# Kernel optimization log

Hardware: AMD Instinct MI355X
Metric: run time of the kernel (lower is better)

## Reference

```python
import jax, jax.numpy as jnp
import numpy as np

N_NODES = 50000
N_EDGES = 800000
N_GRAPHS = 8
IN_CH = 32
HID = 64
EDGE_F = 16
EPS = 1e-5


def setup_inputs() -> dict:
    key = jax.random.key(0)
    ks = jax.random.split(key, 40)
    r = lambda i, shape, s=0.1: (jax.random.normal(ks[i], shape, dtype=jnp.float32) * s)
    inp = {
        "x": jax.random.normal(ks[0], (N_NODES, IN_CH), dtype=jnp.float32),
        "edge_index": jax.random.randint(ks[1], (2, N_EDGES), 0, N_NODES),
        "edge_attr": jax.random.normal(ks[2], (N_EDGES, EDGE_F), dtype=jnp.float32),
        "batch": jnp.sort(jax.random.randint(ks[3], (N_NODES,), 0, N_GRAPHS)),
        "nt_w": r(4, (IN_CH, HID)), "nt_b": jnp.zeros((HID,), jnp.float32),
        "ln0_w": jnp.ones((HID,), jnp.float32), "ln0_b": jnp.zeros((HID,), jnp.float32),
        "c1_wl": r(5, (HID, 2 * HID)), "c1_bl": jnp.zeros((2 * HID,), jnp.float32),
        "c1_wr": r(6, (HID, 2 * HID)), "c1_br": jnp.zeros((2 * HID,), jnp.float32),
        "c1_we": r(7, (EDGE_F, 2 * HID)), "c1_att": r(8, (2, HID)),
        "c1_b": jnp.zeros((2 * HID,), jnp.float32),
        "n1_w": jnp.ones((2 * HID,), jnp.float32), "n1_b": jnp.zeros((2 * HID,), jnp.float32),
        "c2_wl": r(9, (2 * HID, 2 * HID)), "c2_bl": jnp.zeros((2 * HID,), jnp.float32),
        "c2_wr": r(10, (2 * HID, 2 * HID)), "c2_br": jnp.zeros((2 * HID,), jnp.float32),
        "c2_we": r(11, (EDGE_F, 2 * HID)), "c2_att": r(12, (2, HID)),
        "c2_b": jnp.zeros((2 * HID,), jnp.float32),
        "n2_w": jnp.ones((2 * HID,), jnp.float32), "n2_b": jnp.zeros((2 * HID,), jnp.float32),
        "c3_wl": r(13, (2 * HID, HID)), "c3_bl": jnp.zeros((HID,), jnp.float32),
        "c3_wr": r(14, (2 * HID, HID)), "c3_br": jnp.zeros((HID,), jnp.float32),
        "c3_we": r(15, (EDGE_F, HID)), "c3_att": r(16, (1, HID)),
        "c3_b": jnp.zeros((HID,), jnp.float32),
        "pof_w": r(17, (HID, 1)), "pof_b": jnp.zeros((1,), jnp.float32),
        "hp_w": r(18, (HID, 1)), "hp_b": jnp.zeros((1,), jnp.float32),
    }
    return inp


def _layer_norm(x, w, b):
    # torch nn.LayerNorm over last dim
    mu = jnp.mean(x, axis=-1, keepdims=True)
    xc = x - mu
    var = jnp.mean(xc * xc, axis=-1, keepdims=True)
    return xc * jax.lax.rsqrt(var + EPS) * w + b


def _graph_norm(x, w, b):
    # PyG LayerNorm mode='graph' with batch=None: normalize over all nodes+channels
    mu = jnp.mean(x)
    xc = x - mu
    var = jnp.mean(xc * xc)
    return xc * jax.lax.rsqrt(var + EPS) * w + b


def _gatv2(x, src, dst, ea, wl, bl, wr, br, we, att, b, heads, outc):
    n = x.shape[0]
    xl = (x @ wl + bl).reshape(n, heads, outc)   # source transform
    xr = (x @ wr + br).reshape(n, heads, outc)   # target transform
    e = (ea @ we).reshape(-1, heads, outc)       # [E,H,C] edge embedding
    m = jax.nn.leaky_relu(xl[src] + xr[dst] + e, 0.2)  # [E,H,C]
    alpha = jnp.einsum("ehc,hc->eh", m, att)      # [E,H]
    amax = jax.ops.segment_max(alpha, dst, num_segments=n)
    amax = jnp.where(jnp.isfinite(amax), amax, 0.0)
    p = jnp.exp(alpha - amax[dst])
    denom = jax.ops.segment_sum(p, dst, num_segments=n)
    alpha = p / (denom[dst] + 1e-16)
    out = jax.ops.segment_sum(xl[src] * alpha[..., None], dst, num_segments=n)
    return out.reshape(n, heads * outc) + b


def reference(x, edge_index, edge_attr, batch,
              nt_w, nt_b, ln0_w, ln0_b,
              c1_wl, c1_bl, c1_wr, c1_br, c1_we, c1_att, c1_b, n1_w, n1_b,
              c2_wl, c2_bl, c2_wr, c2_br, c2_we, c2_att, c2_b, n2_w, n2_b,
              c3_wl, c3_bl, c3_wr, c3_br, c3_we, c3_att, c3_b,
              pof_w, pof_b, hp_w, hp_b):
    src, dst = edge_index[0], edge_index[1]
    # node_transform (dropout = identity in eval mode)
    h = _layer_norm(jax.nn.elu(x @ nt_w + nt_b), ln0_w, ln0_b)
    h = _gatv2(h, src, dst, edge_attr, c1_wl, c1_bl, c1_wr, c1_br, c1_we, c1_att, c1_b, 2, HID)
    h = jax.nn.elu(_graph_norm(h, n1_w, n1_b))
    h = _gatv2(h, src, dst, edge_attr, c2_wl, c2_bl, c2_wr, c2_br, c2_we, c2_att, c2_b, 2, HID)
    h = jax.nn.elu(_graph_norm(h, n2_w, n2_b))
    h = _gatv2(h, src, dst, edge_attr, c3_wl, c3_bl, c3_wr, c3_br, c3_we, c3_att, c3_b, 1, HID)
    pof_pred = (h @ pof_w + pof_b)[:, 0]
    sums = jax.ops.segment_sum(h, batch, num_segments=N_GRAPHS)
    cnt = jax.ops.segment_sum(jnp.ones((h.shape[0],), h.dtype), batch, num_segments=N_GRAPHS)
    graph_emb = sums / jnp.maximum(cnt, 1.0)[:, None]
    has_pof_pred = (graph_emb @ hp_w + hp_b)[:, 0]
    return pof_pred, has_pof_pred
```

## Files before the change

### kernel.cpp

```cpp
#include <hip/hip_runtime.h>
#include <cstdint>
#include <cstddef>

#define DI __device__ __forceinline__

constexpr int N = 50000;
constexpr int E = 800000;
constexpr int NG = 8;

constexpr size_t AL(size_t x){ return (x + 1023) & ~size_t(1023); }
constexpr size_t OFF_SCAL   = 0;
constexpr size_t OFF_GSUM   = 1024;
constexpr size_t OFF_GCNT   = OFF_GSUM + 2048;
constexpr size_t OFF_DEG    = 4096;
constexpr size_t ZERO_BYTES = OFF_DEG + size_t(N)*4;
constexpr size_t OFF_ROWPTR = AL(ZERO_BYTES);
constexpr size_t OFF_CURSOR = AL(OFF_ROWPTR + size_t(N+1)*4);
constexpr size_t OFF_BSUM   = AL(OFF_CURSOR + size_t(N)*4);
constexpr size_t OFF_BOFF   = AL(OFF_BSUM + 1024);
constexpr size_t OFF_COLSRC = AL(OFF_BOFF + 1024);
constexpr size_t OFF_COLDST = AL(OFF_COLSRC + size_t(E)*4);
constexpr size_t OFF_EAC    = AL(OFF_COLDST + size_t(E)*4);
constexpr size_t OFF_BL     = AL(OFF_EAC + size_t(E)*32);
constexpr size_t OFF_BR     = AL(OFF_BL + size_t(N)*64*4);
constexpr size_t OFF_A      = AL(OFF_BR + size_t(N)*64*4);
constexpr size_t OFF_CACC   = AL(OFF_A + size_t(N)*64*4);
constexpr size_t OFF_DACC   = AL(OFF_CACC + size_t(N)*128*4);
constexpr size_t CACC_ZERO  = (OFF_DACC - OFF_CACC) + size_t(N)*2*4;

template<int START>
DI float wred(float v){
  #pragma unroll
  for (int o = START; o > 0; o >>= 1) v += __shfl_xor(v, o);
  return v;
}

DI float elu(float v){ return v > 0.f ? v : (__expf(v) - 1.f); }

DI uint32_t bfr(float x){ uint32_t u = __float_as_uint(x); return (u + 0x7fffu + ((u >> 16) & 1u)) >> 16; }
DI uint32_t pk2(float a, float b){ return bfr(a) | (bfr(b) << 16); }
DI float lo16(uint32_t u){ return __uint_as_float(u << 16); }
DI float hi16(uint32_t u){ return __uint_as_float(u & 0xffff0000u); }
DI float bf2f(uint16_t u){ return __uint_as_float(uint32_t(u) << 16); }

__global__ void k_deg(const int* __restrict__ ei, int* __restrict__ deg){
  for (int e = blockIdx.x*blockDim.x + threadIdx.x; e < E; e += gridDim.x*blockDim.x)
    atomicAdd(&deg[ei[E + e]], 1);
}

__global__ __launch_bounds__(256) void k_scan1(const int* __restrict__ deg,
                                               int* __restrict__ rowptr,
                                               int* __restrict__ bsum){
  __shared__ int s[256];
  int t = threadIdx.x, i = blockIdx.x*256 + t;
  int v = (i < N) ? deg[i] : 0;
  s[t] = v; __syncthreads();
  for (int off = 1; off < 256; off <<= 1){
    int x = (t >= off) ? s[t-off] : 0;
    __syncthreads();
    s[t] += x; __syncthreads();
  }
  if (i < N) rowptr[i] = s[t] - v;
  if (t == 255) bsum[blockIdx.x] = s[255];
}

__global__ __launch_bounds__(256) void k_scan2(const int* __restrict__ bsum,
                                               int* __restrict__ boff, int nb){
  __shared__ int s[256];
  int t = threadIdx.x;
  int v = (t < nb) ? bsum[t] : 0;
  s[t] = v; __syncthreads();
  for (int off = 1; off < 256; off <<= 1){
    int x = (t >= off) ? s[t-off] : 0;
    __syncthreads();
    s[t] += x; __syncthreads();
  }
  if (t < nb) boff[t] = s[t] - v;
}

__global__ __launch_bounds__(256) void k_scan3(int* __restrict__ rowptr,
                                               const int* __restrict__ boff,
                                               int* __restrict__ cursor){
  int t = threadIdx.x, i = blockIdx.x*256 + t;
  if (i < N){
    int v = rowptr[i] + boff[blockIdx.x];
    rowptr[i] = v;
    cursor[i] = v;
  }
  if (i == 0) rowptr[N] = E;
}

__global__ void k_fill(const int* __restrict__ ei, const float* __restrict__ ea,
                       int* __restrict__ cursor, int* __restrict__ colsrc,
                       int* __restrict__ coldst, uint32_t* __restrict__ eac){
  for (int e = blockIdx.x*blockDim.x + threadIdx.x; e < E; e += gridDim.x*blockDim.x){
    int dn = ei[E + e];
    int pos = atomicAdd(&cursor[dn], 1);
    colsrc[pos] = ei[e];
    coldst[pos] = dn;
    const float4* s = (const float4*)(ea + size_t(e)*16);
    float4 v0 = s[0], v1 = s[1], v2 = s[2], v3 = s[3];
    uint32_t* d8 = eac + size_t(pos)*8;
    d8[0] = pk2(v0.x, v0.y); d8[1] = pk2(v0.z, v0.w);
    d8[2] = pk2(v1.x, v1.y); d8[3] = pk2(v1.z, v1.w);
    d8[4] = pk2(v2.x, v2.y); d8[5] = pk2(v2.z, v2.w);
    d8[6] = pk2(v3.x, v3.y); d8[7] = pk2(v3.z, v3.w);
  }
}

__global__ __launch_bounds__(256) void k_node_transform(
    const float* __restrict__ x, const float* __restrict__ w,
    const float* __restrict__ b, const float* __restrict__ lnw,
    const float* __restrict__ lnb, uint32_t* __restrict__ A){
  int wid = (blockIdx.x*256 + threadIdx.x) >> 6;
  int l = threadIdx.x & 63;
  if (wid >= N) return;
  float xv = x[wid*32 + (l & 31)];
  float acc = b[l];
  #pragma unroll
  for (int k = 0; k < 32; ++k){
    float hk = __shfl(xv, k);
    acc = fmaf(hk, w[k*64 + l], acc);
  }
  float v = elu(acc);
  float mu = wred<32>(v) * (1.f/64.f);
  float xc = v - mu;
  float var = wred<32>(xc*xc) * (1.f/64.f);
  float rs = rsqrtf(var + 1e-5f);
  float o = xc*rs*lnw[l] + lnb[l];
  float partner = __shfl_xor(o, 1);
  if ((l & 1) == 0) A[wid*32 + (l >> 1)] = pk2(o, partner);
}

template<int K, int C>
__global__ __launch_bounds__(256) void k_lin2(
    const uint32_t* __restrict__ h,
    const float* __restrict__ Wl_, const float* __restrict__ bl_,
    const float* __restrict__ Wr_, const float* __restrict__ br_,
    uint32_t* __restrict__ Bl, uint32_t* __restrict__ Br){
  constexpr int CB = 64;
  constexpr int NL = C / CB;
  constexpr int NCB = 2*NL;
  constexpr int NT = 32;
  constexpr int WQ = K / 4;
  __shared__ float Wl[K][CB];
  __shared__ float Hl[NT][K + 4];
  const int tid = threadIdx.x;
  const int cb = blockIdx.x % NCB;
  const int tile0 = blockIdx.x / NCB;
  const int tstep = gridDim.x / NCB;
  const bool left = cb < NL;
  const float* W = left ? Wl_ : Wr_;
  const float* bias = left ? bl_ : br_;
  uint32_t* Out = left ? Bl : Br;
  const int wcb = left ? cb : cb - NL;
  for (int idx = tid; idx < K*CB; idx += 256){
    int k = idx >> 6, c = idx & 63;
    Wl[k][c] = W[k*C + wcb*CB + c];
  }
  const int nl = tid >> 4;
  const int cq = tid & 15;
  const float* bb = bias + wcb*CB + cq*4;
  float4 b4 = make_float4(bb[0], bb[1], bb[2], bb[3]);
  constexpr int NTILES = (N + NT - 1)/NT;
  for (int tile = tile0; tile < NTILES; tile += tstep){
    int n0 = tile*NT;
    __syncthreads();
    for (int idx = tid; idx < NT*WQ; idx += 256){
      int nn = idx / WQ, q = idx % WQ;
      uint2 v = make_uint2(0,0);
      int n = n0 + nn;
      if (n < N) v = ((const uint2*)(h + size_t(n)*(K/2)))[q];
      Hl[nn][4*q]   = lo16(v.x);
      Hl[nn][4*q+1] = hi16(v.x);
      Hl[nn][4*q+2] = lo16(v.y);
      Hl[nn][4*q+3] = hi16(v.y);
    }
    __syncthreads();
    float4 a0 = make_float4(0,0,0,0), a1 = a0;
    #pragma unroll 8
    for (int k = 0; k < K; ++k){
      float4 w4 = ((const float4*)&Wl[k][0])[cq];
      float h0v = Hl[nl][k];
      float h1v = Hl[nl+16][k];
      a0.x = fmaf(h0v, w4.x, a0.x); a0.y = fmaf(h0v, w4.y, a0.y);
      a0.z = fmaf(h0v, w4.z, a0.z); a0.w = fmaf(h0v, w4.w, a0.w);
      a1.x = fmaf(h1v, w4.x, a1.x); a1.y = fmaf(h1v, w4.y, a1.y);
      a1.z = fmaf(h1v, w4.z, a1.z); a1.w = fmaf(h1v, w4.w, a1.w);
    }
    int na = n0 + nl, nb2 = n0 + nl + 16;
    if (na < N){
      uint2 o = make_uint2(pk2(a0.x+b4.x, a0.y+b4.y), pk2(a0.z+b4.z, a0.w+b4.w));
      ((uint2*)(Out + size_t(na)*(C/2)))[wcb*16 + cq] = o;
    }
    if (nb2 < N){
      uint2 o = make_uint2(pk2(a1.x+b4.x, a1.y+b4.y), pk2(a1.z+b4.z, a1.w+b4.w));
      ((uint2*)(Out + size_t(nb2)*(C/2)))[wcb*16 + cq] = o;
    }
  }
}

DI float edge_logit2(float xlx, float xly, float xrx, float xry,
                     const float2* wr_, float2 at2, uint4 qa, uint4 qb){
  float c0 = xlx + xrx, c1 = xly + xry;
  uint32_t wq[8] = {qa.x,qa.y,qa.z,qa.w, qb.x,qb.y,qb.z,qb.w};
  #pragma unroll
  for (int k = 0; k < 8; ++k){
    float e0 = lo16(wq[k]), e1 = hi16(wq[k]);
    c0 = fmaf(e0, wr_[2*k].x, c0);   c1 = fmaf(e0, wr_[2*k].y, c1);
    c0 = fmaf(e1, wr_[2*k+1].x, c0); c1 = fmaf(e1, wr_[2*k+1].y, c1);
  }
  c0 = c0 > 0.f ? c0 : 0.2f*c0;
  c1 = c1 > 0.f ? c1 : 0.2f*c1;
  return wred<16>(c0*at2.x + c1*at2.y);
}

DI float edge_logit1(float xl, float xr, const float* wr_, float at,
                     uint4 qa, uint4 qb){
  float c0 = xl + xr;
  uint32_t wq[8] = {qa.x,qa.y,qa.z,qa.w, qb.x,qb.y,qb.z,qb.w};
  #pragma unroll
  for (int k = 0; k < 8; ++k){
    float e0 = lo16(wq[k]), e1 = hi16(wq[k]);
    c0 = fmaf(e0, wr_[2*k], c0);
    c0 = fmaf(e1, wr_[2*k+1], c0);
  }
  c0 = c0 > 0.f ? c0 : 0.2f*c0;
  return wred<32>(c0*at);
}

constexpr int CHUNK = 32;
constexpr int NCHUNK = E / CHUNK;

template<int H>
__global__ __launch_bounds__(256, 4) void k_attagg(
    const uint32_t* __restrict__ Bl, const uint32_t* __restrict__ Br,
    const float* __restrict__ we, const float* __restrict__ att,
    const uint32_t* __restrict__ eac,
    const int* __restrict__ colsrc, const int* __restrict__ coldst,
    float* __restrict__ Cacc, float* __restrict__ Dacc){
  const int tid = threadIdx.x;
  const int l = tid & 63;
  const int g = (blockIdx.x*256 + tid) >> 6;
  if (g >= NCHUNK) return;
  const int e0 = g*CHUNK;
  const uint4* eb = (const uint4*)eac;
  const int cs = colsrc[e0 + (l & 31)];
  const int cd = coldst[e0 + (l & 31)];
  if constexpr (H == 2){
    float2 wr_[16];
    const float2* we2 = (const float2*)we;
    #pragma unroll
    for (int k = 0; k < 16; ++k) wr_[k] = we2[k*64 + l];
    const float2 at2 = ((const float2*)att)[l];
    int cur = __shfl(cd, 0);
    uint32_t xrw = Br[size_t(cur)*64 + l];
    float d = 0.f, a0 = 0.f, a1 = 0.f;
    #pragma unroll 1
    for (int jb = 0; jb < CHUNK; jb += 4){
      int s0 = __shfl(cs, jb),   s1 = __shfl(cs, jb+1);
      int s2 = __shfl(cs, jb+2), s3 = __shfl(cs, jb+3);
      uint32_t x0 = Bl[size_t(s0)*64 + l];
      uint32_t x1 = Bl[size_t(s1)*64 + l];
      uint32_t x2 = Bl[size_t(s2)*64 + l];
      uint32_t x3 = Bl[size_t(s3)*64 + l];
      const uint4* q = eb + size_t(e0 + jb)*2;
      uint4 qa0 = q[0], qb0 = q[1], qa1 = q[2], qb1 = q[3];
      uint4 qa2 = q[4], qb2 = q[5], qa3 = q[6], qb3 = q[7];
      int d0 = __shfl(cd, jb),   d1 = __shfl(cd, jb+1);
      int d2 = __shfl(cd, jb+2), d3 = __shfl(cd, jb+3);
      #define FLUSH2(dn) { \
        atomicAdd(&Cacc[size_t(cur)*128 + 2*l],   a0); \
        atomicAdd(&Cacc[size_t(cur)*128 + 2*l+1], a1); \
        if (l == 0)  atomicAdd(&Dacc[cur*2],   d); \
        if (l == 32) atomicAdd(&Dacc[cur*2+1], d); \
        cur = dn; xrw = Br[size_t(cur)*64 + l]; d = a0 = a1 = 0.f; }
      #define EDGE2(xk, qak, qbk) { \
        float t = edge_logit2(lo16(xk), hi16(xk), lo16(xrw), hi16(xrw), wr_, at2, qak, qbk); \
        float p = __expf(t); d += p; \
        a0 = fmaf(p, lo16(xk), a0); a1 = fmaf(p, hi16(xk), a1); }
      if (d0 != cur) FLUSH2(d0); EDGE2(x0, qa0, qb0);
      if (d1 != cur) FLUSH2(d1); EDGE2(x1, qa1, qb1);
      if (d2 != cur) FLUSH2(d2); EDGE2(x2, qa2, qb2);
      if (d3 != cur) FLUSH2(d3); EDGE2(x3, qa3, qb3);
      #undef FLUSH2
      #undef EDGE2
    }
    atomicAdd(&Cacc[size_t(cur)*128 + 2*l],   a0);
    atomicAdd(&Cacc[size_t(cur)*128 + 2*l+1], a1);
    if (l == 0)  atomicAdd(&Dacc[cur*2],   d);
    if (l == 32) atomicAdd(&Dacc[cur*2+1], d);
  } else {
    float wr_[16];
    #pragma unroll
    for (int k = 0; k < 16; ++k) wr_[k] = we[k*64 + l];
    const float at = att[l];
    const uint16_t* Bl16 = (const uint16_t*)Bl;
    const uint16_t* Br16 = (const uint16_t*)Br;
    int cur = __shfl(cd, 0);
    float xr = bf2f(Br16[size_t(cur)*64 + l]);
    float d = 0.f, a0 = 0.f;
    #pragma unroll 1
    for (int jb = 0; jb < CHUNK; jb += 4){
      int s0 = __shfl(cs, jb),   s1 = __shfl(cs, jb+1);
      int s2 = __shfl(cs, jb+2), s3 = __shfl(cs, jb+3);
      float x0 = bf2f(Bl16[size_t(s0)*64 + l]);
      float x1 = bf2f(Bl16[size_t(s1)*64 + l]);
      float x2 = bf2f(Bl16[size_t(s2)*64 + l]);
      float x3 = bf2f(Bl16[size_t(s3)*64 + l]);
      const uint4* q = eb + size_t(e0 + jb)*2;
      uint4 qa0 = q[0], qb0 = q[1], qa1 = q[2], qb1 = q[3];
      uint4 qa2 = q[4], qb2 = q[5], qa3 = q[6], qb3 = q[7];
      int d0 = __shfl(cd, jb),   d1 = __shfl(cd, jb+1);
      int d2 = __shfl(cd, jb+2), d3 = __shfl(cd, jb+3);
      #define FLUSH1(dn) { \
        atomicAdd(&Cacc[size_t(cur)*64 + l], a0); \
        if (l == 0) atomicAdd(&Dacc[cur], d); \
        cur = dn; xr = bf2f(Br16[size_t(cur)*64 + l]); d = a0 = 0.f; }
      #define EDGE1(xk, qak, qbk) { \
        float t = edge_logit1(xk, xr, wr_, at, qak, qbk); \
        float p = __expf(t); d += p; a0 = fmaf(p, xk, a0); }
      if (d0 != cur) FLUSH1(d0); EDGE1(x0, qa0, qb0);
      if (d1 != cur) FLUSH1(d1); EDGE1(x1, qa1, qb1);
      if (d2 != cur) FLUSH1(d2); EDGE1(x2, qa2, qb2);
      if (d3 != cur) FLUSH1(d3); EDGE1(x3, qa3, qb3);
      #undef FLUSH1
      #undef EDGE1
    }
    atomicAdd(&Cacc[size_t(cur)*64 + l], a0);
    if (l == 0) atomicAdd(&Dacc[cur], d);
  }
}

template<bool GN>
__global__ __launch_bounds__(256) void k_finish2(
    const float* __restrict__ Cacc, const float* __restrict__ Dacc,
    const float* __restrict__ bias, uint32_t* __restrict__ A,
    double* __restrict__ scal){
  float s1p = 0.f, s2p = 0.f;
  for (int i = blockIdx.x*256 + threadIdx.x; i < N*64; i += gridDim.x*256){
    int n = i >> 6, w = i & 63;
    float inv = 1.f/(Dacc[n*2 + (w >> 5)] + 1e-16f);
    float o0 = Cacc[size_t(n)*128 + 2*w]   * inv + bias[2*w];
    float o1 = Cacc[size_t(n)*128 + 2*w+1] * inv + bias[2*w+1];
    A[i] = pk2(o0, o1);
    if constexpr (GN){ s1p += o0 + o1; s2p += o0*o0 + o1*o1; }
  }
  if constexpr (GN){
    float s = wred<32>(s1p), s2 = wred<32>(s2p);
    __shared__ float bs[4], bs2[4];
    int w = threadIdx.x >> 6;
    if ((threadIdx.x & 63) == 0){ bs[w] = s; bs2[w] = s2; }
    __syncthreads();
    if (threadIdx.x == 0){
      double ts  = (double)bs[0] + (double)bs[1] + (double)bs[2] + (double)bs[3];
      double ts2 = (double)bs2[0] + (double)bs2[1] + (double)bs2[2] + (double)bs2[3];
      atomicAdd(&scal[0], ts);
      atomicAdd(&scal[1], ts2);
    }
  }
}

__global__ __launch_bounds__(256) void k_finish1(
    float* __restrict__ Cacc, const float* __restrict__ Dacc,
    const float* __restrict__ bias){
  int i = blockIdx.x*256 + threadIdx.x;
  if (i < N*64){
    int n = i >> 6, c = i & 63;
    Cacc[i] = Cacc[i]/(Dacc[n] + 1e-16f) + bias[c];
  }
}

__global__ __launch_bounds__(256) void k_gn_apply(
    uint32_t* __restrict__ A, const double* __restrict__ scal,
    const float* __restrict__ w, const float* __restrict__ b){
  const double invM = 1.0 / (double(N)*128.0);
  double mu_d = scal[0]*invM;
  double ex2  = scal[1]*invM;
  float mu = (float)mu_d;
  float var = (float)(ex2 - mu_d*mu_d);
  float rs = rsqrtf(var + 1e-5f);
  int i = blockIdx.x*256 + threadIdx.x;
  if (i < N*64){
    int wo = i & 63;
    float2 wv = ((const float2*)w)[wo];
    float2 bv = ((const float2*)b)[wo];
    uint32_t u = A[i];
    float o0 = elu((lo16(u) - mu)*rs*wv.x + bv.x);
    float o1 = elu((hi16(u) - mu)*rs*wv.y + bv.y);
    A[i] = pk2(o0, o1);
  }
}

__global__ __launch_bounds__(256) void k_pool(
    const float* __restrict__ h3, const int* __restrict__ batch,
    const float* __restrict__ pw, const float* __restrict__ pb,
    float* __restrict__ outv, float* __restrict__ gsum, float* __restrict__ gcnt){
  __shared__ float ls[512];
  __shared__ float lc[8];
  int tid = threadIdx.x;
  if (tid < 8) lc[tid] = 0.f;
  for (int i = tid; i < 512; i += 256) ls[i] = 0.f;
  __syncthreads();
  int l = tid & 63;
  int wid = (blockIdx.x*256 + tid) >> 6;
  int NW = (gridDim.x*256) >> 6;
  float pwl = pw[l];
  for (int n = wid; n < N; n += NW){
    float v = h3[size_t(n)*64 + l];
    float pp = wred<32>(v*pwl);
    if (l == 0) outv[n] = pp + pb[0];
    int g = batch[n];
    atomicAdd(&ls[g*64 + l], v);
    if (l == 0) atomicAdd(&lc[g], 1.f);
  }
  __syncthreads();
  for (int i = tid; i < 512; i += 256) atomicAdd(&gsum[i], ls[i]);
  if (tid < 8) atomicAdd(&gcnt[tid], lc[tid]);
}

__global__ __launch_bounds__(512) void k_head(
    const float* __restrict__ gsum, const float* __restrict__ gcnt,
    const float* __restrict__ hw, const float* __restrict__ hb,
    float* __restrict__ outv){
  int g = threadIdx.x >> 6, l = threadIdx.x & 63;
  float cnt = fmaxf(gcnt[g], 1.f);
  float emb = gsum[g*64 + l] / cnt;
  float p = wred<32>(emb*hw[l]);
  if (l == 0) outv[N + g] = p + hb[0];
}

extern "C" void kernel_launch(void* const* d_in, const int* in_sizes, int n_in,
                              void* d_out, int out_size, void* d_ws, size_t ws_size,
                              hipStream_t stream){
  const float* x      = (const float*)d_in[0];
  const int*   ei     = (const int*)  d_in[1];
  const float* ea     = (const float*)d_in[2];
  const int*   batch  = (const int*)  d_in[3];
  const float* nt_w   = (const float*)d_in[4];
  const float* nt_b   = (const float*)d_in[5];
  const float* ln0_w  = (const float*)d_in[6];
  const float* ln0_b  = (const float*)d_in[7];
  const float* c1_wl  = (const float*)d_in[8];
  const float* c1_bl  = (const float*)d_in[9];
  const float* c1_wr  = (const float*)d_in[10];
  const float* c1_br  = (const float*)d_in[11];
  const float* c1_we  = (const float*)d_in[12];
  const float* c1_att = (const float*)d_in[13];
  const float* c1_b   = (const float*)d_in[14];
  const float* n1_w   = (const float*)d_in[15];
  const float* n1_b   = (const float*)d_in[16];
  const float* c2_wl  = (const float*)d_in[17];
  const float* c2_bl  = (const float*)d_in[18];
  const float* c2_wr  = (const float*)d_in[19];
  const float* c2_br  = (const float*)d_in[20];
  const float* c2_we  = (const float*)d_in[21];
  const float* c2_att = (const float*)d_in[22];
  const float* c2_b   = (const float*)d_in[23];
  const float* n2_w   = (const float*)d_in[24];
  const float* n2_b   = (const float*)d_in[25];
  const float* c3_wl  = (const float*)d_in[26];
  const float* c3_bl  = (const float*)d_in[27];
  const float* c3_wr  = (const float*)d_in[28];
  const float* c3_br  = (const float*)d_in[29];
  const float* c3_we  = (const float*)d_in[30];
  const float* c3_att = (const float*)d_in[31];
  const float* c3_b   = (const float*)d_in[32];
  const float* pof_w  = (const float*)d_in[33];
  const float* pof_b  = (const float*)d_in[34];
  const float* hp_w   = (const float*)d_in[35];
  const float* hp_b   = (const float*)d_in[36];
  float* out = (float*)d_out;

  char* w = (char*)d_ws;
  double* scal    = (double*)(w + OFF_SCAL);
  float* gsum     = (float*)(w + OFF_GSUM);
  float* gcnt     = (float*)(w + OFF_GCNT);
  int* deg        = (int*)(w + OFF_DEG);
  int* rowptr     = (int*)(w + OFF_ROWPTR);
  int* cursor     = (int*)(w + OFF_CURSOR);
  int* bsum       = (int*)(w + OFF_BSUM);
  int* boff       = (int*)(w + OFF_BOFF);
  int* colsrc     = (int*)(w + OFF_COLSRC);
  int* coldst     = (int*)(w + OFF_COLDST);
  uint32_t* eac   = (uint32_t*)(w + OFF_EAC);
  uint32_t* Bl    = (uint32_t*)(w + OFF_BL);
  uint32_t* Br    = (uint32_t*)(w + OFF_BR);
  uint32_t* A     = (uint32_t*)(w + OFF_A);
  float* Cacc     = (float*)(w + OFF_CACC);
  float* Dacc     = (float*)(w + OFF_DACC);

  hipMemsetAsync(d_ws, 0, ZERO_BYTES, stream);

  k_deg  <<<1024, 256, 0, stream>>>(ei, deg);
  k_scan1<<<196,  256, 0, stream>>>(deg, rowptr, bsum);
  k_scan2<<<1,    256, 0, stream>>>(bsum, boff, 196);
  k_scan3<<<196,  256, 0, stream>>>(rowptr, boff, cursor);
  k_fill <<<1024, 256, 0, stream>>>(ei, ea, cursor, colsrc, coldst, eac);

  k_node_transform<<<12500, 256, 0, stream>>>(x, nt_w, nt_b, ln0_w, ln0_b, A);

  hipMemsetAsync(w + OFF_CACC, 0, CACC_ZERO, stream);
  k_lin2<64,128><<<2048, 256, 0, stream>>>(A, c1_wl, c1_bl, c1_wr, c1_br, Bl, Br);
  k_attagg<2><<<6250, 256, 0, stream>>>(Bl, Br, c1_we, c1_att, eac, colsrc, coldst, Cacc, Dacc);
  k_finish2<true><<<608, 256, 0, stream>>>(Cacc, Dacc, c1_b, A, scal);
  k_gn_apply<<<12500, 256, 0, stream>>>(A, scal, n1_w, n1_b);

  hipMemsetAsync(w + OFF_CACC, 0, CACC_ZERO, stream);
  k_lin2<128,128><<<2048, 256, 0, stream>>>(A, c2_wl, c2_bl, c2_wr, c2_br, Bl, Br);
  k_attagg<2><<<6250, 256, 0, stream>>>(Bl, Br, c2_we, c2_att, eac, colsrc, coldst, Cacc, Dacc);
  k_finish2<true><<<608, 256, 0, stream>>>(Cacc, Dacc, c2_b, A, scal + 2);
  k_gn_apply<<<12500, 256, 0, stream>>>(A, scal + 2, n2_w, n2_b);

  hipMemsetAsync(w + OFF_CACC, 0, CACC_ZERO, stream);
  k_lin2<128,64><<<1024, 256, 0, stream>>>(A, c3_wl, c3_bl, c3_wr, c3_br, Bl, Br);
  k_attagg<1><<<6250, 256, 0, stream>>>(Bl, Br, c3_we, c3_att, eac, colsrc, coldst, Cacc, Dacc);
  k_finish1<<<12500, 256, 0, stream>>>(Cacc, Dacc, c3_b);

  k_pool<<<512, 256, 0, stream>>>(Cacc, batch, pof_w, pof_b, out, gsum, gcnt);
  k_head<<<1, 512, 0, stream>>>(gsum, gcnt, hp_w, hp_b, out);
}
```

Measured before the change: 746.5 us.

## Switch intermediate storage from bf16 to fp16 and use packed dot2 for edge logits

Replaces the hand-rolled bf16 packing with fp16 via the hardware pkrtz conversion everywhere intermediates are stored. The edge-feature projection in the attention kernels now uses the v_dot2 fp16 instruction with the edge weights pre-packed as half pairs, which halves the FMA count and the weight registers. The attention kernel's launch bounds occupancy hint also rises from 4 to 6. fp16 has a narrower range than bf16 and round-toward-zero packing adds error, and node values that exceed the fp16 range could overflow.

```diff
diff --git a/kernel.cpp b/kernel.cpp
--- a/kernel.cpp
+++ b/kernel.cpp
@@ -37,11 +37,26 @@
 
 DI float elu(float v){ return v > 0.f ? v : (__expf(v) - 1.f); }
 
-DI uint32_t bfr(float x){ uint32_t u = __float_as_uint(x); return (u + 0x7fffu + ((u >> 16) & 1u)) >> 16; }
-DI uint32_t pk2(float a, float b){ return bfr(a) | (bfr(b) << 16); }
-DI float lo16(uint32_t u){ return __uint_as_float(u << 16); }
-DI float hi16(uint32_t u){ return __uint_as_float(u & 0xffff0000u); }
-DI float bf2f(uint16_t u){ return __uint_as_float(uint32_t(u) << 16); }
+typedef __attribute__((ext_vector_type(2))) __fp16 h2v;
+
+DI uint32_t pkh(float a, float b){
+  auto r = __builtin_amdgcn_cvt_pkrtz(a, b);
+  return __builtin_bit_cast(uint32_t, r);
+}
+DI float hlo(uint32_t u){ h2v h = __builtin_bit_cast(h2v, u); return (float)h.x; }
+DI float hhi(uint32_t u){ h2v h = __builtin_bit_cast(h2v, u); return (float)h.y; }
+DI float h2f(uint16_t u){ __fp16 h = __builtin_bit_cast(__fp16, u); return (float)h; }
+
+#if __has_builtin(__builtin_amdgcn_fdot2)
+DI float dot2(uint32_t a, uint32_t b, float c){
+  return __builtin_amdgcn_fdot2(__builtin_bit_cast(h2v, a),
+                                __builtin_bit_cast(h2v, b), c, false);
+}
+#else
+DI float dot2(uint32_t a, uint32_t b, float c){
+  return fmaf(hlo(a), hlo(b), fmaf(hhi(a), hhi(b), c));
+}
+#endif
 
 __global__ void k_deg(const int* __restrict__ ei, int* __restrict__ deg){
   for (int e = blockIdx.x*blockDim.x + threadIdx.x; e < E; e += gridDim.x*blockDim.x)
@@ -101,10 +116,10 @@
     const float4* s = (const float4*)(ea + size_t(e)*16);
     float4 v0 = s[0], v1 = s[1], v2 = s[2], v3 = s[3];
     uint32_t* d8 = eac + size_t(pos)*8;
-    d8[0] = pk2(v0.x, v0.y); d8[1] = pk2(v0.z, v0.w);
-    d8[2] = pk2(v1.x, v1.y); d8[3] = pk2(v1.z, v1.w);
-    d8[4] = pk2(v2.x, v2.y); d8[5] = pk2(v2.z, v2.w);
-    d8[6] = pk2(v3.x, v3.y); d8[7] = pk2(v3.z, v3.w);
+    d8[0] = pkh(v0.x, v0.y); d8[1] = pkh(v0.z, v0.w);
+    d8[2] = pkh(v1.x, v1.y); d8[3] = pkh(v1.z, v1.w);
+    d8[4] = pkh(v2.x, v2.y); d8[5] = pkh(v2.z, v2.w);
+    d8[6] = pkh(v3.x, v3.y); d8[7] = pkh(v3.z, v3.w);
   }
 }
 
@@ -129,7 +144,7 @@
   float rs = rsqrtf(var + 1e-5f);
   float o = xc*rs*lnw[l] + lnb[l];
   float partner = __shfl_xor(o, 1);
-  if ((l & 1) == 0) A[wid*32 + (l >> 1)] = pk2(o, partner);
+  if ((l & 1) == 0) A[wid*32 + (l >> 1)] = pkh(o, partner);
 }
 
 template<int K, int C>
@@ -171,10 +186,10 @@
       uint2 v = make_uint2(0,0);
       int n = n0 + nn;
       if (n < N) v = ((const uint2*)(h + size_t(n)*(K/2)))[q];
-      Hl[nn][4*q]   = lo16(v.x);
-      Hl[nn][4*q+1] = hi16(v.x);
-      Hl[nn][4*q+2] = lo16(v.y);
-      Hl[nn][4*q+3] = hi16(v.y);
+      Hl[nn][4*q]   = hlo(v.x);
+      Hl[nn][4*q+1] = hhi(v.x);
+      Hl[nn][4*q+2] = hlo(v.y);
+      Hl[nn][4*q+3] = hhi(v.y);
     }
     __syncthreads();
     float4 a0 = make_float4(0,0,0,0), a1 = a0;
@@ -190,41 +205,37 @@
     }
     int na = n0 + nl, nb2 = n0 + nl + 16;
     if (na < N){
-      uint2 o = make_uint2(pk2(a0.x+b4.x, a0.y+b4.y), pk2(a0.z+b4.z, a0.w+b4.w));
+      uint2 o = make_uint2(pkh(a0.x+b4.x, a0.y+b4.y), pkh(a0.z+b4.z, a0.w+b4.w));
       ((uint2*)(Out + size_t(na)*(C/2)))[wcb*16 + cq] = o;
     }
     if (nb2 < N){
-      uint2 o = make_uint2(pk2(a1.x+b4.x, a1.y+b4.y), pk2(a1.z+b4.z, a1.w+b4.w));
+      uint2 o = make_uint2(pkh(a1.x+b4.x, a1.y+b4.y), pkh(a1.z+b4.z, a1.w+b4.w));
       ((uint2*)(Out + size_t(nb2)*(C/2)))[wcb*16 + cq] = o;
     }
   }
 }
 
 DI float edge_logit2(float xlx, float xly, float xrx, float xry,
-                     const float2* wr_, float2 at2, uint4 qa, uint4 qb){
+                     const uint32_t* wp0, const uint32_t* wp1, float2 at2,
+                     uint4 qa, uint4 qb){
   float c0 = xlx + xrx, c1 = xly + xry;
   uint32_t wq[8] = {qa.x,qa.y,qa.z,qa.w, qb.x,qb.y,qb.z,qb.w};
   #pragma unroll
   for (int k = 0; k < 8; ++k){
-    float e0 = lo16(wq[k]), e1 = hi16(wq[k]);
-    c0 = fmaf(e0, wr_[2*k].x, c0);   c1 = fmaf(e0, wr_[2*k].y, c1);
-    c0 = fmaf(e1, wr_[2*k+1].x, c0); c1 = fmaf(e1, wr_[2*k+1].y, c1);
+    c0 = dot2(wq[k], wp0[k], c0);
+    c1 = dot2(wq[k], wp1[k], c1);
   }
   c0 = c0 > 0.f ? c0 : 0.2f*c0;
   c1 = c1 > 0.f ? c1 : 0.2f*c1;
   return wred<16>(c0*at2.x + c1*at2.y);
 }
 
-DI float edge_logit1(float xl, float xr, const float* wr_, float at,
+DI float edge_logit1(float xl, float xr, const uint32_t* wp, float at,
                      uint4 qa, uint4 qb){
   float c0 = xl + xr;
   uint32_t wq[8] = {qa.x,qa.y,qa.z,qa.w, qb.x,qb.y,qb.z,qb.w};
   #pragma unroll
-  for (int k = 0; k < 8; ++k){
-    float e0 = lo16(wq[k]), e1 = hi16(wq[k]);
-    c0 = fmaf(e0, wr_[2*k], c0);
-    c0 = fmaf(e1, wr_[2*k+1], c0);
-  }
+  for (int k = 0; k < 8; ++k) c0 = dot2(wq[k], wp[k], c0);
   c0 = c0 > 0.f ? c0 : 0.2f*c0;
   return wred<32>(c0*at);
 }
@@ -233,7 +244,7 @@
 constexpr int NCHUNK = E / CHUNK;
 
 template<int H>
-__global__ __launch_bounds__(256, 4) void k_attagg(
+__global__ __launch_bounds__(256, 6) void k_attagg(
     const uint32_t* __restrict__ Bl, const uint32_t* __restrict__ Br,
     const float* __restrict__ we, const float* __restrict__ att,
     const uint32_t* __restrict__ eac,
@@ -248,13 +259,16 @@
   const int cs = colsrc[e0 + (l & 31)];
   const int cd = coldst[e0 + (l & 31)];
   if constexpr (H == 2){
-    float2 wr_[16];
-    const float2* we2 = (const float2*)we;
+    uint32_t wp0[8], wp1[8];
     #pragma unroll
-    for (int k = 0; k < 16; ++k) wr_[k] = we2[k*64 + l];
+    for (int k = 0; k < 8; ++k){
+      wp0[k] = pkh(we[(2*k)*128 + 2*l],   we[(2*k+1)*128 + 2*l]);
+      wp1[k] = pkh(we[(2*k)*128 + 2*l+1], we[(2*k+1)*128 + 2*l+1]);
+    }
     const float2 at2 = ((const float2*)att)[l];
     int cur = __shfl(cd, 0);
     uint32_t xrw = Br[size_t(cur)*64 + l];
+    float xrx = hlo(xrw), xry = hhi(xrw);
     float d = 0.f, a0 = 0.f, a1 = 0.f;
     #pragma unroll 1
     for (int jb = 0; jb < CHUNK; jb += 4){
@@ -274,11 +288,12 @@
         atomicAdd(&Cacc[size_t(cur)*128 + 2*l+1], a1); \
         if (l == 0)  atomicAdd(&Dacc[cur*2],   d); \
         if (l == 32) atomicAdd(&Dacc[cur*2+1], d); \
-        cur = dn; xrw = Br[size_t(cur)*64 + l]; d = a0 = a1 = 0.f; }
+        cur = dn; xrw = Br[size_t(cur)*64 + l]; \
+        xrx = hlo(xrw); xry = hhi(xrw); d = a0 = a1 = 0.f; }
       #define EDGE2(xk, qak, qbk) { \
-        float t = edge_logit2(lo16(xk), hi16(xk), lo16(xrw), hi16(xrw), wr_, at2, qak, qbk); \
+        float t = edge_logit2(hlo(xk), hhi(xk), xrx, xry, wp0, wp1, at2, qak, qbk); \
         float p = __expf(t); d += p; \
-        a0 = fmaf(p, lo16(xk), a0); a1 = fmaf(p, hi16(xk), a1); }
+        a0 = fmaf(p, hlo(xk), a0); a1 = fmaf(p, hhi(xk), a1); }
       if (d0 != cur) FLUSH2(d0); EDGE2(x0, qa0, qb0);
       if (d1 != cur) FLUSH2(d1); EDGE2(x1, qa1, qb1);
       if (d2 != cur) FLUSH2(d2); EDGE2(x2, qa2, qb2);
@@ -291,23 +306,24 @@
     if (l == 0)  atomicAdd(&Dacc[cur*2],   d);
     if (l == 32) atomicAdd(&Dacc[cur*2+1], d);
   } else {
-    float wr_[16];
+    uint32_t wp[8];
     #pragma unroll
-    for (int k = 0; k < 16; ++k) wr_[k] = we[k*64 + l];
+    for (int k = 0; k < 8; ++k)
+      wp[k] = pkh(we[(2*k)*64 + l], we[(2*k+1)*64 + l]);
     const float at = att[l];
     const uint16_t* Bl16 = (const uint16_t*)Bl;
     const uint16_t* Br16 = (const uint16_t*)Br;
     int cur = __shfl(cd, 0);
-    float xr = bf2f(Br16[size_t(cur)*64 + l]);
+    float xr = h2f(Br16[size_t(cur)*64 + l]);
     float d = 0.f, a0 = 0.f;
     #pragma unroll 1
     for (int jb = 0; jb < CHUNK; jb += 4){
       int s0 = __shfl(cs, jb),   s1 = __shfl(cs, jb+1);
       int s2 = __shfl(cs, jb+2), s3 = __shfl(cs, jb+3);
-      float x0 = bf2f(Bl16[size_t(s0)*64 + l]);
-      float x1 = bf2f(Bl16[size_t(s1)*64 + l]);
-      float x2 = bf2f(Bl16[size_t(s2)*64 + l]);
-      float x3 = bf2f(Bl16[size_t(s3)*64 + l]);
+      float x0 = h2f(Bl16[size_t(s0)*64 + l]);
+      float x1 = h2f(Bl16[size_t(s1)*64 + l]);
+      float x2 = h2f(Bl16[size_t(s2)*64 + l]);
+      float x3 = h2f(Bl16[size_t(s3)*64 + l]);
       const uint4* q = eb + size_t(e0 + jb)*2;
       uint4 qa0 = q[0], qb0 = q[1], qa1 = q[2], qb1 = q[3];
       uint4 qa2 = q[4], qb2 = q[5], qa3 = q[6], qb3 = q[7];
@@ -316,9 +332,9 @@
       #define FLUSH1(dn) { \
         atomicAdd(&Cacc[size_t(cur)*64 + l], a0); \
         if (l == 0) atomicAdd(&Dacc[cur], d); \
-        cur = dn; xr = bf2f(Br16[size_t(cur)*64 + l]); d = a0 = 0.f; }
+        cur = dn; xr = h2f(Br16[size_t(cur)*64 + l]); d = a0 = 0.f; }
       #define EDGE1(xk, qak, qbk) { \
-        float t = edge_logit1(xk, xr, wr_, at, qak, qbk); \
+        float t = edge_logit1(xk, xr, wp, at, qak, qbk); \
         float p = __expf(t); d += p; a0 = fmaf(p, xk, a0); }
       if (d0 != cur) FLUSH1(d0); EDGE1(x0, qa0, qb0);
       if (d1 != cur) FLUSH1(d1); EDGE1(x1, qa1, qb1);
@@ -343,7 +359,7 @@
     float inv = 1.f/(Dacc[n*2 + (w >> 5)] + 1e-16f);
     float o0 = Cacc[size_t(n)*128 + 2*w]   * inv + bias[2*w];
     float o1 = Cacc[size_t(n)*128 + 2*w+1] * inv + bias[2*w+1];
-    A[i] = pk2(o0, o1);
+    A[i] = pkh(o0, o1);
     if constexpr (GN){ s1p += o0 + o1; s2p += o0*o0 + o1*o1; }
   }
   if constexpr (GN){
@@ -386,9 +402,9 @@
     float2 wv = ((const float2*)w)[wo];
     float2 bv = ((const float2*)b)[wo];
     uint32_t u = A[i];
-    float o0 = elu((lo16(u) - mu)*rs*wv.x + bv.x);
-    float o1 = elu((hi16(u) - mu)*rs*wv.y + bv.y);
-    A[i] = pk2(o0, o1);
+    float o0 = elu((hlo(u) - mu)*rs*wv.x + bv.x);
+    float o1 = elu((hhi(u) - mu)*rs*wv.y + bv.y);
+    A[i] = pkh(o0, o1);
   }
 }
 
```

Measured after the change: 661.3 us. 1.13x faster.
